# Performance work log

Measured on AMD Instinct MI355X. Metric: run time of the kernel, lower is better.

## Reference

```python
import jax, jax.numpy as jnp
import numpy as np

TEMPERATURE = 1.0
IGNORE_INDEX = -100


def setup_inputs() -> dict:
    key = jax.random.key(0)
    k1, k2, k3 = jax.random.split(key, 3)
    N, V = 8192, 32000
    Q, D = 8192, 512
    return {
        "input": jax.random.normal(k1, (N, V), dtype=jnp.float32),
        "label": jax.random.randint(k2, (N,), 0, V, dtype=jnp.int64),
        "query": jax.random.normal(k3, (Q, D), dtype=jnp.float32),
    }


def _cross_entropy(logits, label):
    # nn.CrossEntropyLoss(ignore_index=IGNORE_INDEX): mean NLL over non-ignored.
    logp = jax.nn.log_softmax(logits, axis=-1)
    safe_label = jnp.clip(label, 0, logits.shape[-1] - 1)
    nll = -jnp.take_along_axis(logp, safe_label[:, None], axis=-1)[:, 0]
    valid = (label != IGNORE_INDEX)
    num_valid = jnp.maximum(jnp.sum(valid), 1)
    return jnp.sum(jnp.where(valid, nll, 0.0)) / num_valid.astype(logits.dtype)


def _query_similarity_penalty(query, temperature):
    sq_norm = jnp.sum(query * query, axis=-1)  # [Q]
    sq = sq_norm[:, None] + sq_norm[None, :] - 2.0 * (query @ query.T)
    sq = jnp.maximum(sq, 0.0)
    dist = jnp.sqrt(jnp.where(sq > 0.0, sq, 1.0))
    dist = jnp.where(sq > 0.0, dist, 0.0)  # exact 0 on diagonal
    sim = jnp.exp(-dist / temperature)
    return jnp.sqrt(jnp.sum(sim * sim))  # Frobenius norm


def reference(input, label, query):
    ce = _cross_entropy(input, label)
    penalty = _query_similarity_penalty(query, TEMPERATURE)
    return ce + penalty
```

## Files before the change

### kernel.cpp

```cpp
#include <hip/hip_runtime.h>
#include <hip/hip_bf16.h>
#include <cstdint>

typedef unsigned short u16;
typedef __attribute__((ext_vector_type(8))) short short8;
typedef __attribute__((ext_vector_type(4))) float floatx4;

#define IGNORE_INDEX (-100)

__global__ __launch_bounds__(64) void init_acc(float* acc) {
    if (threadIdx.x < 3) acc[threadIdx.x] = 0.f;
}

__global__ __launch_bounds__(256) void prep_kernel(const float* __restrict__ q,
                                                   u16* __restrict__ qb,
                                                   float* __restrict__ nrm) {
    const int gwave = (blockIdx.x * 256 + threadIdx.x) >> 6;
    const int lane  = threadIdx.x & 63;
    const float4* src = (const float4*)(q + (size_t)gwave * 512);
    float4 a = src[lane * 2];
    float4 b = src[lane * 2 + 1];
    float v[8] = {a.x, a.y, a.z, a.w, b.x, b.y, b.z, b.w};
    float ss = 0.f;
    union { u16 u[8]; uint4 p; } pk;
#pragma unroll
    for (int t = 0; t < 8; ++t) {
        ss += v[t] * v[t];
        __hip_bfloat16 h = __float2bfloat16(v[t]);
        pk.u[t] = *(u16*)&h;
    }
    ((uint4*)qb)[(size_t)gwave * 64 + lane] = pk.p;
#pragma unroll
    for (int off = 32; off; off >>= 1) ss += __shfl_down(ss, off);
    if (lane == 0) nrm[gwave] = ss;
}

#define GLD16(g, l) __builtin_amdgcn_global_load_lds(                          \
    (const __attribute__((address_space(1))) void*)(g),                        \
    (__attribute__((address_space(3))) void*)(l), 16, 0, 0)

__global__ __launch_bounds__(256, 2) void fused_kernel(const u16* __restrict__ qb,
                                                       const float* __restrict__ nrm,
                                                       const float* __restrict__ x,
                                                       const int* __restrict__ lab,
                                                       float* __restrict__ accs,
                                                       int V, int N, int tiles_per_side) {
    __shared__ __align__(16) u16 At[128 * 64];
    __shared__ __align__(16) u16 Bt[128 * 64];
    __shared__ float red[4];
    const int bid  = blockIdx.x;
    const int tid  = threadIdx.x;
    const int lane = tid & 63;
    const int w    = tid >> 6;

    if (bid % 5 == 0) {
        int t = bid / 5;
        int ti = 0, rem = t;
        while (rem >= tiles_per_side - ti) { rem -= tiles_per_side - ti; ++ti; }
        const int tj = ti + rem;
        const int i0 = ti * 128;
        const int j0 = tj * 128;
        const int wr = w >> 1, wc = w & 1;
        const int m15 = lane & 15, quad = lane >> 4;

        floatx4 acc[4][4];
#pragma unroll
        for (int a = 0; a < 4; ++a)
#pragma unroll
            for (int b = 0; b < 4; ++b) acc[a][b] = (floatx4)0.f;

        for (int kt = 0; kt < 8; ++kt) {
            const int k0 = kt * 64;
#pragma unroll
            for (int it = 0; it < 4; ++it) {
                int c   = it * 256 + tid;
                int row = c >> 3;
                int kc  = (c & 7) ^ (row & 7);
                const u16* ga = qb + (size_t)(i0 + row) * 512 + k0 + kc * 8;
                const u16* gb = qb + (size_t)(j0 + row) * 512 + k0 + kc * 8;
                GLD16(ga, &At[c * 8]);
                GLD16(gb, &Bt[c * 8]);
            }
            __syncthreads();
#pragma unroll
            for (int ks = 0; ks < 2; ++ks) {
                const int kcq = ks * 4 + quad;
                short8 af[4], bfr[4];
#pragma unroll
                for (int f = 0; f < 4; ++f) {
                    int ra = wr * 64 + f * 16 + m15;
                    af[f]  = *(const short8*)&At[(ra * 8 + (kcq ^ (ra & 7))) * 8];
                    int rb = wc * 64 + f * 16 + m15;
                    bfr[f] = *(const short8*)&Bt[(rb * 8 + (kcq ^ (rb & 7))) * 8];
                }
#pragma unroll
                for (int fi = 0; fi < 4; ++fi)
#pragma unroll
                    for (int fj = 0; fj < 4; ++fj)
                        acc[fi][fj] = __builtin_amdgcn_mfma_f32_16x16x32_bf16(
                            af[fi], bfr[fj], acc[fi][fj], 0, 0, 0);
            }
            __syncthreads();
        }

        float ni[4][4], nj[4];
#pragma unroll
        for (int fi = 0; fi < 4; ++fi)
#pragma unroll
            for (int r = 0; r < 4; ++r)
                ni[fi][r] = nrm[i0 + wr * 64 + fi * 16 + quad * 4 + r];
#pragma unroll
        for (int fj = 0; fj < 4; ++fj) nj[fj] = nrm[j0 + wc * 64 + fj * 16 + m15];

        float lsum = 0.f;
#pragma unroll
        for (int fi = 0; fi < 4; ++fi) {
#pragma unroll
            for (int fj = 0; fj < 4; ++fj) {
#pragma unroll
                for (int r = 0; r < 4; ++r) {
                    int i = i0 + wr * 64 + fi * 16 + quad * 4 + r;
                    int j = j0 + wc * 64 + fj * 16 + m15;
                    float sq = ni[fi][r] + nj[fj] - 2.f * acc[fi][fj][r];
                    float s;
                    if (i == j) s = 1.f;
                    else if (sq > 0.f) s = __expf(-sqrtf(sq));
                    else s = 1.f;
                    lsum += s * s;
                }
            }
        }
#pragma unroll
        for (int off = 32; off; off >>= 1) lsum += __shfl_down(lsum, off);
        if (lane == 0) red[w] = lsum;
        __syncthreads();
        if (tid == 0) {
            const float wgt = (ti == tj) ? 1.f : 2.f;
            atomicAdd(&accs[0], wgt * (red[0] + red[1] + red[2] + red[3]));
        }
    } else {
        const int row = bid - bid / 5 - 1;
        if (row >= N) return;
        const float* xr = x + (size_t)row * V;

        int l = 0; float xl = 0.f;
        if (tid == 0) {
            l = lab[row];
            if (l != IGNORE_INDEX) xl = xr[l];
        }

        const int nvec = V >> 2;
        const floatx4* __restrict__ xv = (const floatx4*)xr;
        float s0 = 0.f, s1 = 0.f, s2 = 0.f, s3 = 0.f;
        int idx = tid;
        const int lim = nvec - 256 * 7;
        for (; idx < lim; idx += 256 * 8) {
            floatx4 v[8];
#pragma unroll
            for (int u = 0; u < 8; ++u)
                v[u] = __builtin_nontemporal_load(xv + idx + 256 * u);
#pragma unroll
            for (int u = 0; u < 8; ++u) {
                s0 += __expf(v[u].x);
                s1 += __expf(v[u].y);
                s2 += __expf(v[u].z);
                s3 += __expf(v[u].w);
            }
        }
        for (; idx < nvec; idx += 256) {
            floatx4 v = __builtin_nontemporal_load(xv + idx);
            s0 += __expf(v.x); s1 += __expf(v.y); s2 += __expf(v.z); s3 += __expf(v.w);
        }
        for (int t2 = (nvec << 2) + tid; t2 < V; t2 += 256)
            s0 += __expf(xr[t2]);
        float s = (s0 + s1) + (s2 + s3);
#pragma unroll
        for (int off = 32; off; off >>= 1) s += __shfl_down(s, off);
        if (lane == 0) red[w] = s;
        __syncthreads();
        if (tid == 0) {
            float S = red[0] + red[1] + red[2] + red[3];
            if (l != IGNORE_INDEX) {
                atomicAdd(&accs[1], __logf(S) - xl);
                atomicAdd(&accs[2], 1.f);
            }
        }
    }
}

__global__ void finalize_kernel(const float* __restrict__ accs, float* __restrict__ out) {
    out[0] = accs[1] / fmaxf(accs[2], 1.f) + sqrtf(accs[0]);
}

extern "C" void kernel_launch(void* const* d_in, const int* in_sizes, int n_in,
                              void* d_out, int out_size, void* d_ws, size_t ws_size,
                              hipStream_t stream) {
    const float* input = (const float*)d_in[0];
    const int*   label = (const int*)d_in[1];
    const float* query = (const float*)d_in[2];
    float* out = (float*)d_out;

    const int N = in_sizes[1];
    const int V = in_sizes[0] / N;
    const int D = 512;
    const int Q = in_sizes[2] / D;
    const int T = Q / 128;
    const int U = T * (T + 1) / 2;

    float* accs = (float*)d_ws;
    float* nrm  = (float*)((char*)d_ws + 4096);
    u16*   qb   = (u16*)  ((char*)d_ws + 4096 + 64 * 1024);

    hipLaunchKernelGGL(init_acc, dim3(1), dim3(64), 0, stream, accs);
    hipLaunchKernelGGL(prep_kernel, dim3(Q / 4), dim3(256), 0, stream, query, qb, nrm);
    hipLaunchKernelGGL(fused_kernel, dim3(U * 5), dim3(256), 0, stream,
                       qb, nrm, input, label, accs, V, N, T);
    hipLaunchKernelGGL(finalize_kernel, dim3(1), dim3(1), 0, stream, accs, out);
}
```

Baseline: 1.413 ms.

## Spread atomics across slots, rotate row read start, raise occupancy hint

Replaces the three global atomic accumulators with 64 strided slots per quantity, reduced by a 64-thread finalize kernel, to cut contention on single addresses. Each cross-entropy row now starts its read at a row-dependent rotated offset, so concurrent rows do not hit the same memory channels together. Launch bounds move from 2 to 3 blocks per CU. The costs are extra index arithmetic and predication in the tail loop, plus register pressure from the tighter occupancy bound on the MFMA path.

```diff
diff --git a/kernel.cpp b/kernel.cpp
--- a/kernel.cpp
+++ b/kernel.cpp
@@ -8,8 +8,12 @@
 
 #define IGNORE_INDEX (-100)
 
-__global__ __launch_bounds__(64) void init_acc(float* acc) {
-    if (threadIdx.x < 3) acc[threadIdx.x] = 0.f;
+#define SIM_OFF 64
+#define NLL_OFF 320
+#define CNT_OFF 576
+
+__global__ __launch_bounds__(256) void init_acc(float* acc) {
+    for (int i = threadIdx.x; i < 1024; i += 256) acc[i] = 0.f;
 }
 
 __global__ __launch_bounds__(256) void prep_kernel(const float* __restrict__ q,
@@ -39,7 +43,7 @@
     (const __attribute__((address_space(1))) void*)(g),                        \
     (__attribute__((address_space(3))) void*)(l), 16, 0, 0)
 
-__global__ __launch_bounds__(256, 2) void fused_kernel(const u16* __restrict__ qb,
+__global__ __launch_bounds__(256, 3) void fused_kernel(const u16* __restrict__ qb,
                                                        const float* __restrict__ nrm,
                                                        const float* __restrict__ x,
                                                        const int* __restrict__ lab,
@@ -52,6 +56,7 @@
     const int tid  = threadIdx.x;
     const int lane = tid & 63;
     const int w    = tid >> 6;
+    const int slot = (bid & 63) * 4;
 
     if (bid % 5 == 0) {
         int t = bid / 5;
@@ -136,7 +141,7 @@
         __syncthreads();
         if (tid == 0) {
             const float wgt = (ti == tj) ? 1.f : 2.f;
-            atomicAdd(&accs[0], wgt * (red[0] + red[1] + red[2] + red[3]));
+            atomicAdd(&accs[SIM_OFF + slot], wgt * (red[0] + red[1] + red[2] + red[3]));
         }
     } else {
         const int row = bid - bid / 5 - 1;
@@ -151,14 +156,18 @@
 
         const int nvec = V >> 2;
         const floatx4* __restrict__ xv = (const floatx4*)xr;
+        const int rot = (row * 787) % nvec;
         float s0 = 0.f, s1 = 0.f, s2 = 0.f, s3 = 0.f;
-        int idx = tid;
-        const int lim = nvec - 256 * 7;
-        for (; idx < lim; idx += 256 * 8) {
+
+        const int nfull = nvec / 2048;
+        for (int k = 0; k < nfull; ++k) {
             floatx4 v[8];
 #pragma unroll
-            for (int u = 0; u < 8; ++u)
-                v[u] = __builtin_nontemporal_load(xv + idx + 256 * u);
+            for (int u = 0; u < 8; ++u) {
+                int vi = k * 2048 + u * 256 + tid;
+                int r  = vi + rot; if (r >= nvec) r -= nvec;
+                v[u] = __builtin_nontemporal_load(xv + r);
+            }
 #pragma unroll
             for (int u = 0; u < 8; ++u) {
                 s0 += __expf(v[u].x);
@@ -167,12 +176,35 @@
                 s3 += __expf(v[u].w);
             }
         }
-        for (; idx < nvec; idx += 256) {
-            floatx4 v = __builtin_nontemporal_load(xv + idx);
-            s0 += __expf(v.x); s1 += __expf(v.y); s2 += __expf(v.z); s3 += __expf(v.w);
-        }
-        for (int t2 = (nvec << 2) + tid; t2 < V; t2 += 256)
-            s0 += __expf(xr[t2]);
+        {
+            const int base = nfull * 2048;
+            floatx4 v[8];
+#pragma unroll
+            for (int u = 0; u < 8; ++u) {
+                int vb = base + u * 256;
+                if (vb < nvec) {
+                    int vi = vb + tid;
+                    int r  = vi + rot;
+                    if (r >= nvec) r -= nvec;
+                    if (r >= nvec) r -= nvec;
+                    v[u] = __builtin_nontemporal_load(xv + r);
+                } else v[u] = (floatx4)0.f;
+            }
+#pragma unroll
+            for (int u = 0; u < 8; ++u) {
+                int vb = base + u * 256;
+                if (vb < nvec) {
+                    int vi = vb + tid;
+                    float e0 = __expf(v[u].x), e1 = __expf(v[u].y);
+                    float e2 = __expf(v[u].z), e3 = __expf(v[u].w);
+                    bool ok = vi < nvec;
+                    s0 += ok ? e0 : 0.f;
+                    s1 += ok ? e1 : 0.f;
+                    s2 += ok ? e2 : 0.f;
+                    s3 += ok ? e3 : 0.f;
+                }
+            }
+        }
         float s = (s0 + s1) + (s2 + s3);
 #pragma unroll
         for (int off = 32; off; off >>= 1) s += __shfl_down(s, off);
@@ -181,15 +213,26 @@
         if (tid == 0) {
             float S = red[0] + red[1] + red[2] + red[3];
             if (l != IGNORE_INDEX) {
-                atomicAdd(&accs[1], __logf(S) - xl);
-                atomicAdd(&accs[2], 1.f);
+                atomicAdd(&accs[NLL_OFF + slot], __logf(S) - xl);
+                atomicAdd(&accs[CNT_OFF + slot], 1.f);
             }
         }
     }
 }
 
-__global__ void finalize_kernel(const float* __restrict__ accs, float* __restrict__ out) {
-    out[0] = accs[1] / fmaxf(accs[2], 1.f) + sqrtf(accs[0]);
+__global__ __launch_bounds__(64) void finalize_kernel(const float* __restrict__ accs,
+                                                      float* __restrict__ out) {
+    const int t = threadIdx.x;
+    float sim = accs[SIM_OFF + t * 4];
+    float nll = accs[NLL_OFF + t * 4];
+    float cnt = accs[CNT_OFF + t * 4];
+#pragma unroll
+    for (int off = 32; off; off >>= 1) {
+        sim += __shfl_down(sim, off);
+        nll += __shfl_down(nll, off);
+        cnt += __shfl_down(cnt, off);
+    }
+    if (t == 0) out[0] = nll / fmaxf(cnt, 1.f) + sqrtf(sim);
 }
 
 extern "C" void kernel_launch(void* const* d_in, const int* in_sizes, int n_in,
@@ -211,9 +254,9 @@
     float* nrm  = (float*)((char*)d_ws + 4096);
     u16*   qb   = (u16*)  ((char*)d_ws + 4096 + 64 * 1024);
 
-    hipLaunchKernelGGL(init_acc, dim3(1), dim3(64), 0, stream, accs);
+    hipLaunchKernelGGL(init_acc, dim3(1), dim3(256), 0, stream, accs);
     hipLaunchKernelGGL(prep_kernel, dim3(Q / 4), dim3(256), 0, stream, query, qb, nrm);
     hipLaunchKernelGGL(fused_kernel, dim3(U * 5), dim3(256), 0, stream,
                        qb, nrm, input, label, accs, V, N, T);
-    hipLaunchKernelGGL(finalize_kernel, dim3(1), dim3(1), 0, stream, accs, out);
-}
+    hipLaunchKernelGGL(finalize_kernel, dim3(1), dim3(64), 0, stream, accs, out);
+}
```

Measured after the change: 1.285 ms. 1.1x faster.
